# Optimization experiments

Measured on AMD Instinct MI355X. Metric: run time of the kernel, lower is better.

## Reference

```python
import jax, jax.numpy as jnp
import numpy as np

NUM_HEADS = 16
D_K = 8  # == n_qubits


def setup_inputs() -> dict:
    key = jax.random.key(0)
    k1, k2, k3 = jax.random.split(key, 3)
    x = jax.random.normal(k1, (4, 2048, 128), dtype=jnp.float32)
    # trainable RX angles, one per qubit (tq.RX has_params=True)
    theta = jax.random.normal(k2, (D_K,), dtype=jnp.float32)
    # out_proj: Linear(embed_dim, embed_dim, bias=False)
    w_out = jax.random.normal(k3, (128, 128), dtype=jnp.float32) * (1.0 / np.sqrt(128.0))
    return {"x": x, "theta": theta, "w_out": w_out}


def quantum_features(x, theta):
    # x: [b, s, e]. Per head of size d_k: encode RX(x_i), trainable RX(theta_i)
    # (composes to RX(x_i + theta_i)), CNOT ladder [i, i+1], measure PauliZ.
    # Heisenberg picture: Z_w -> Z_0...Z_w, so <Z_w> = prod_{i<=w} cos(x_i + theta_i).
    b, s, e = x.shape
    heads = x.reshape(b, s, NUM_HEADS, D_K)
    return jnp.cumprod(jnp.cos(heads + theta), axis=-1)  # [b, s, h, d_k]


def reference(x, theta, w_out):
    b, s, e = x.shape
    # q == k == v: same shared q_layer applied to the same x three times.
    qkv = quantum_features(x, theta)            # [b, s, h, d_k]
    q = qkv.transpose(0, 2, 1, 3)               # [b, h, s, d_k]
    scores = jnp.einsum('bhqd,bhkd->bhqk', q, q) / np.sqrt(D_K)
    attn = jax.nn.softmax(scores, axis=-1)      # dropout is identity at eval
    out = jnp.einsum('bhqk,bhkd->bhqd', attn, q)
    out = out.transpose(0, 2, 1, 3).reshape(b, s, e)
    return out @ w_out.T
```

## Files before the change

kernel.cpp:

```cpp
#include <hip/hip_runtime.h>

#define BATCH 4
#define SEQ   2048
#define EMB   128
#define NH    16
#define DK    8

#define QSCALE 0.510069726f

typedef _Float16 v2h __attribute__((ext_vector_type(2)));
typedef _Float16 v4h __attribute__((ext_vector_type(4)));
typedef __fp16   v2fp __attribute__((ext_vector_type(2)));
typedef float    v4f __attribute__((ext_vector_type(4)));

#define CHUNK  512
#define NCHUNK (SEQ / CHUNK)
#define VTP    520

__launch_bounds__(512, 8)
__global__ void attn_kernel(const float* __restrict__ x,
                            const float* __restrict__ theta,
                            _Float16* __restrict__ Ah ) {
  __shared__ __align__(16) _Float16 Kl[CHUNK * 8];
  __shared__ __align__(16) _Float16 VT[16][VTP];

  const int tid  = threadIdx.x;
  const int L    = tid & 63;
  const int quad = L >> 4;
  const int ln   = L & 15;
  const int wv   = tid >> 6;
  const int bh     = blockIdx.x >> 4;
  const int qchunk = blockIdx.x & 15;
  const int qb     = qchunk * 128 + wv * 16;
  const int b = bh >> 4;
  const int h = bh & 15;

  float th[DK];
#pragma unroll
  for (int i = 0; i < DK; ++i) th[i] = theta[i];

  for (int i = tid; i < 8 * VTP / 4; i += 512) {
    v4h v = (i < VTP / 4) ? (v4h){(_Float16)1.f, (_Float16)1.f,
                                  (_Float16)1.f, (_Float16)1.f}
                          : (v4h){0, 0, 0, 0};
    *(v4h*)(&VT[8][0] + i * 4) = v;
  }

  const int c0 = qchunk >> 2;
  v4h qf = {0, 0, 0, 0};
  v4f acc = (v4f){0.f, 0.f, 0.f, 0.f};
  const v4f zf = (v4f){0.f, 0.f, 0.f, 0.f};

  for (int cc = 0; cc < NCHUNK; ++cc) {
    const int c = (c0 + cc) & (NCHUNK - 1);
    if (cc) __syncthreads();

    {
      const float* xp = x + ((size_t)b * SEQ + c * CHUNK + tid) * EMB + h * DK;
      const float4 a0 = *(const float4*)(xp);
      const float4 a1 = *(const float4*)(xp + 4);

      float r[8];
      r[0] = __cosf(a0.x + th[0]);
      r[1] = r[0] * __cosf(a0.y + th[1]);
      r[2] = r[1] * __cosf(a0.z + th[2]);
      r[3] = r[2] * __cosf(a0.w + th[3]);
      r[4] = r[3] * __cosf(a1.x + th[4]);
      r[5] = r[4] * __cosf(a1.y + th[5]);
      r[6] = r[5] * __cosf(a1.z + th[6]);
      r[7] = r[6] * __cosf(a1.w + th[7]);

      _Float16 hv[8];
#pragma unroll
      for (int i = 0; i < 8; ++i) hv[i] = (_Float16)r[i];

      union { v4h v[2]; float4 f; } u;
      u.v[0] = (v4h){hv[0], hv[1], hv[2], hv[3]};
      u.v[1] = (v4h){hv[4], hv[5], hv[6], hv[7]};
      *(float4*)&Kl[tid * 8] = u.f;

#pragma unroll
      for (int d = 0; d < 8; ++d) VT[d][tid] = hv[d];
    }
    __syncthreads();

    if (cc == 0) {
      const v4h qsc = {(_Float16)QSCALE, (_Float16)QSCALE,
                       (_Float16)QSCALE, (_Float16)QSCALE};
      const int lrow = qb - c0 * CHUNK + ln;
      if (quad < 2) qf = *(const v4h*)&Kl[lrow * 8 + quad * 4] * qsc;
    }

    for (int t16 = 0; t16 < CHUNK / 16; ++t16) {
      const v4h kv = *(const v4h*)&Kl[(t16 * 16 + ln) * 8 + (quad & 1) * 4];
      const v4h kf = (quad < 2) ? kv : (v4h){0, 0, 0, 0};
      const v4h vt = *(const v4h*)&VT[ln][t16 * 16 + quad * 4];
      const v4f s = __builtin_amdgcn_mfma_f32_16x16x16f16(kf, qf, zf, 0, 0, 0);
      union { v2fp p[2]; v4h v; } pk;
      pk.p[0] = __builtin_amdgcn_cvt_pkrtz(__builtin_amdgcn_exp2f(s[0]),
                                           __builtin_amdgcn_exp2f(s[1]));
      pk.p[1] = __builtin_amdgcn_cvt_pkrtz(__builtin_amdgcn_exp2f(s[2]),
                                           __builtin_amdgcn_exp2f(s[3]));
      acc = __builtin_amdgcn_mfma_f32_16x16x16f16(vt, pk.v, acc, 0, 0, 0);
    }
  }

  {
    const float den = __shfl(acc[0], 32 + ln, 64);
    const float inv = 1.0f / den;
    if (quad < 2) {
      const int qrow = qb + ln;
      v4h o = {(_Float16)(acc[0] * inv), (_Float16)(acc[1] * inv),
               (_Float16)(acc[2] * inv), (_Float16)(acc[3] * inv)};
      *(v4h*)(Ah + ((size_t)b * SEQ + qrow) * EMB + h * DK + quad * 4) = o;
    }
  }
}

__launch_bounds__(256, 4)
__global__ void proj_kernel(const _Float16* __restrict__ Ah,
                            const float* __restrict__ W,
                            float* __restrict__ out) {
  __shared__ __align__(16) _Float16 Ahs[64][136];
  __shared__ __align__(16) _Float16 Whs[64][136];

  const int tid  = threadIdx.x;
  const int L    = tid & 63;
  const int wv   = tid >> 6;
  const int quad = L >> 4;
  const int ln   = L & 15;
  const int rowbase = blockIdx.x * 64;
  const int colbase = blockIdx.y * 64;

#pragma unroll
  for (int it = 0; it < 4; ++it) {
    const int idx = it * 256 + tid;
    const int r  = idx >> 4;
    const int c8 = idx & 15;
    *(uint4*)&Ahs[r][c8 * 8] =
        *(const uint4*)(Ah + (size_t)(rowbase + r) * EMB + c8 * 8);
  }
#pragma unroll
  for (int it = 0; it < 8; ++it) {
    const int idx = it * 256 + tid;
    const int n  = idx >> 5;
    const int c4 = idx & 31;
    const float4 w = *(const float4*)(W + (size_t)(colbase + n) * EMB + c4 * 4);
    v4h wh = {(_Float16)w.x, (_Float16)w.y, (_Float16)w.z, (_Float16)w.w};
    *(v4h*)&Whs[n][c4 * 4] = wh;
  }
  __syncthreads();

  v4f acc[4];
#pragma unroll
  for (int nt = 0; nt < 4; ++nt) acc[nt] = (v4f){0.f, 0.f, 0.f, 0.f};

#pragma unroll
  for (int k8 = 0; k8 < 8; ++k8) {
    const v4h af = *(const v4h*)&Ahs[wv * 16 + ln][k8 * 16 + quad * 4];
#pragma unroll
    for (int nt = 0; nt < 4; ++nt) {
      const v4h bf = *(const v4h*)&Whs[nt * 16 + ln][k8 * 16 + quad * 4];
      acc[nt] = __builtin_amdgcn_mfma_f32_16x16x16f16(af, bf, acc[nt], 0, 0, 0);
    }
  }

#pragma unroll
  for (int nt = 0; nt < 4; ++nt) {
    const int col = colbase + nt * 16 + ln;
#pragma unroll
    for (int r = 0; r < 4; ++r) {
      out[(size_t)(rowbase + wv * 16 + quad * 4 + r) * EMB + col] = acc[nt][r];
    }
  }
}

extern "C" void kernel_launch(void* const* d_in, const int* in_sizes, int n_in,
                              void* d_out, int out_size, void* d_ws, size_t ws_size,
                              hipStream_t stream) {
  const float* x     = (const float*)d_in[0];
  const float* theta = (const float*)d_in[1];
  const float* w_out = (const float*)d_in[2];
  float* out = (float*)d_out;

  _Float16* Ah = (_Float16*)d_ws;

  attn_kernel<<<dim3(1024), dim3(512), 0, stream>>>(x, theta, Ah);

  proj_kernel<<<dim3((BATCH * SEQ) / 64, 2), dim3(256), 0, stream>>>(Ah, w_out, out);
}
```

Baseline: 95.92 us.

## Split attention key range across two blocks with partial-sum reduce kernel

The attention kernel now splits the key sequence into two halves, each handled by a separate 256-thread block. Each wave processes two 16-row query tiles so that K/V fragments are reused, and the next chunk's x is prefetched into registers while the current chunk is computed. Unnormalised partial numerators and denominators are written in fp32 to a workspace, and a new reduce kernel combines the two halves and normalises before the projection. This adds an extra launch and extra global traffic in exchange for more blocks and better MFMA reuse per key load.

```diff
diff --git a/kernel.cpp b/kernel.cpp
--- a/kernel.cpp
+++ b/kernel.cpp
@@ -13,25 +13,29 @@
 typedef __fp16   v2fp __attribute__((ext_vector_type(2)));
 typedef float    v4f __attribute__((ext_vector_type(4)));
 
-#define CHUNK  512
-#define NCHUNK (SEQ / CHUNK)
-#define VTP    520
-
-__launch_bounds__(512, 8)
+#define CHUNK  256
+#define NCH    4
+#define VTPAD  264
+#define NROW   (BATCH * SEQ)
+#define NHROW  (BATCH * NH * SEQ)
+#define PSTR   12
+
+__launch_bounds__(256, 8)
 __global__ void attn_kernel(const float* __restrict__ x,
                             const float* __restrict__ theta,
-                            _Float16* __restrict__ Ah ) {
+                            float* __restrict__ Pp ) {
   __shared__ __align__(16) _Float16 Kl[CHUNK * 8];
-  __shared__ __align__(16) _Float16 VT[16][VTP];
+  __shared__ __align__(16) _Float16 VT[16][VTPAD];
 
   const int tid  = threadIdx.x;
   const int L    = tid & 63;
   const int quad = L >> 4;
   const int ln   = L & 15;
   const int wv   = tid >> 6;
-  const int bh     = blockIdx.x >> 4;
-  const int qchunk = blockIdx.x & 15;
-  const int qb     = qchunk * 128 + wv * 16;
+  const int bh     = blockIdx.x >> 5;
+  const int qchunk = (blockIdx.x >> 1) & 15;
+  const int split  = blockIdx.x & 1;
+  const int qb     = qchunk * 128 + wv * 32;
   const int b = bh >> 4;
   const int h = bh & 15;
 
@@ -39,27 +43,21 @@
 #pragma unroll
   for (int i = 0; i < DK; ++i) th[i] = theta[i];
 
-  for (int i = tid; i < 8 * VTP / 4; i += 512) {
-    v4h v = (i < VTP / 4) ? (v4h){(_Float16)1.f, (_Float16)1.f,
-                                  (_Float16)1.f, (_Float16)1.f}
-                          : (v4h){0, 0, 0, 0};
+  for (int i = tid; i < 8 * VTPAD / 4; i += 256) {
+    v4h v = (i < VTPAD / 4) ? (v4h){(_Float16)1.f, (_Float16)1.f,
+                                    (_Float16)1.f, (_Float16)1.f}
+                            : (v4h){0, 0, 0, 0};
     *(v4h*)(&VT[8][0] + i * 4) = v;
   }
 
-  const int c0 = qchunk >> 2;
-  v4h qf = {0, 0, 0, 0};
-  v4f acc = (v4f){0.f, 0.f, 0.f, 0.f};
-  const v4f zf = (v4f){0.f, 0.f, 0.f, 0.f};
-
-  for (int cc = 0; cc < NCHUNK; ++cc) {
-    const int c = (c0 + cc) & (NCHUNK - 1);
-    if (cc) __syncthreads();
-
-    {
-      const float* xp = x + ((size_t)b * SEQ + c * CHUNK + tid) * EMB + h * DK;
-      const float4 a0 = *(const float4*)(xp);
-      const float4 a1 = *(const float4*)(xp + 4);
-
+  v4h qf[2] = {{0, 0, 0, 0}, {0, 0, 0, 0}};
+  if (quad < 2) {
+#pragma unroll
+    for (int t = 0; t < 2; ++t) {
+      const int qrow = qb + t * 16 + ln;
+      const float* xq = x + ((size_t)b * SEQ + qrow) * EMB + h * DK;
+      const float4 a0 = *(const float4*)(xq);
+      const float4 a1 = *(const float4*)(xq + 4);
       float r[8];
       r[0] = __cosf(a0.x + th[0]);
       r[1] = r[0] * __cosf(a0.y + th[1]);
@@ -69,52 +67,109 @@
       r[5] = r[4] * __cosf(a1.y + th[5]);
       r[6] = r[5] * __cosf(a1.z + th[6]);
       r[7] = r[6] * __cosf(a1.w + th[7]);
-
+      qf[t] = (v4h){(_Float16)(r[quad * 4 + 0] * QSCALE),
+                    (_Float16)(r[quad * 4 + 1] * QSCALE),
+                    (_Float16)(r[quad * 4 + 2] * QSCALE),
+                    (_Float16)(r[quad * 4 + 3] * QSCALE)};
+    }
+  }
+
+  const float* xb = x + (size_t)b * SEQ * EMB + h * DK;
+  const int cbase = split * NCH;
+  float4 pa0, pa1;
+  {
+    const float* xp = xb + (size_t)(cbase * CHUNK + tid) * EMB;
+    pa0 = *(const float4*)(xp);
+    pa1 = *(const float4*)(xp + 4);
+  }
+
+  v4f acc[2];
+  acc[0] = (v4f){0.f, 0.f, 0.f, 0.f};
+  acc[1] = (v4f){0.f, 0.f, 0.f, 0.f};
+  const v4f zf = (v4f){0.f, 0.f, 0.f, 0.f};
+
+  for (int cc = 0; cc < NCH; ++cc) {
+    {
+      float r[8];
+      r[0] = __cosf(pa0.x + th[0]);
+      r[1] = r[0] * __cosf(pa0.y + th[1]);
+      r[2] = r[1] * __cosf(pa0.z + th[2]);
+      r[3] = r[2] * __cosf(pa0.w + th[3]);
+      r[4] = r[3] * __cosf(pa1.x + th[4]);
+      r[5] = r[4] * __cosf(pa1.y + th[5]);
+      r[6] = r[5] * __cosf(pa1.z + th[6]);
+      r[7] = r[6] * __cosf(pa1.w + th[7]);
       _Float16 hv[8];
 #pragma unroll
       for (int i = 0; i < 8; ++i) hv[i] = (_Float16)r[i];
-
       union { v4h v[2]; float4 f; } u;
       u.v[0] = (v4h){hv[0], hv[1], hv[2], hv[3]};
       u.v[1] = (v4h){hv[4], hv[5], hv[6], hv[7]};
       *(float4*)&Kl[tid * 8] = u.f;
-
 #pragma unroll
       for (int d = 0; d < 8; ++d) VT[d][tid] = hv[d];
     }
     __syncthreads();
 
-    if (cc == 0) {
-      const v4h qsc = {(_Float16)QSCALE, (_Float16)QSCALE,
-                       (_Float16)QSCALE, (_Float16)QSCALE};
-      const int lrow = qb - c0 * CHUNK + ln;
-      if (quad < 2) qf = *(const v4h*)&Kl[lrow * 8 + quad * 4] * qsc;
+    if (cc + 1 < NCH) {
+      const float* xp = xb + (size_t)((cbase + cc + 1) * CHUNK + tid) * EMB;
+      pa0 = *(const float4*)(xp);
+      pa1 = *(const float4*)(xp + 4);
     }
 
     for (int t16 = 0; t16 < CHUNK / 16; ++t16) {
-      const v4h kv = *(const v4h*)&Kl[(t16 * 16 + ln) * 8 + (quad & 1) * 4];
-      const v4h kf = (quad < 2) ? kv : (v4h){0, 0, 0, 0};
+      const v4h kf = *(const v4h*)&Kl[(t16 * 16 + ln) * 8 + (quad & 1) * 4];
       const v4h vt = *(const v4h*)&VT[ln][t16 * 16 + quad * 4];
-      const v4f s = __builtin_amdgcn_mfma_f32_16x16x16f16(kf, qf, zf, 0, 0, 0);
-      union { v2fp p[2]; v4h v; } pk;
-      pk.p[0] = __builtin_amdgcn_cvt_pkrtz(__builtin_amdgcn_exp2f(s[0]),
-                                           __builtin_amdgcn_exp2f(s[1]));
-      pk.p[1] = __builtin_amdgcn_cvt_pkrtz(__builtin_amdgcn_exp2f(s[2]),
-                                           __builtin_amdgcn_exp2f(s[3]));
-      acc = __builtin_amdgcn_mfma_f32_16x16x16f16(vt, pk.v, acc, 0, 0, 0);
-    }
-  }
-
-  {
-    const float den = __shfl(acc[0], 32 + ln, 64);
-    const float inv = 1.0f / den;
+#pragma unroll
+      for (int t = 0; t < 2; ++t) {
+        const v4f s = __builtin_amdgcn_mfma_f32_16x16x16f16(kf, qf[t], zf, 0, 0, 0);
+        union { v2fp p[2]; v4h v; } pk;
+        pk.p[0] = __builtin_amdgcn_cvt_pkrtz(__builtin_amdgcn_exp2f(s[0]),
+                                             __builtin_amdgcn_exp2f(s[1]));
+        pk.p[1] = __builtin_amdgcn_cvt_pkrtz(__builtin_amdgcn_exp2f(s[2]),
+                                             __builtin_amdgcn_exp2f(s[3]));
+        acc[t] = __builtin_amdgcn_mfma_f32_16x16x16f16(vt, pk.v, acc[t], 0, 0, 0);
+      }
+    }
+    __syncthreads();
+  }
+
+  float* pb = Pp + ((size_t)split * NHROW + (size_t)bh * SEQ) * PSTR;
+#pragma unroll
+  for (int t = 0; t < 2; ++t) {
+    const int qrow = qb + t * 16 + ln;
     if (quad < 2) {
-      const int qrow = qb + ln;
-      v4h o = {(_Float16)(acc[0] * inv), (_Float16)(acc[1] * inv),
-               (_Float16)(acc[2] * inv), (_Float16)(acc[3] * inv)};
-      *(v4h*)(Ah + ((size_t)b * SEQ + qrow) * EMB + h * DK + quad * 4) = o;
-    }
-  }
+      float4 st = make_float4(acc[t][0], acc[t][1], acc[t][2], acc[t][3]);
+      *(float4*)(pb + (size_t)qrow * PSTR + quad * 4) = st;
+    } else if (quad == 2) {
+      pb[(size_t)qrow * PSTR + 8] = acc[t][0];
+    }
+  }
+}
+
+__global__ void reduce_kernel(const float* __restrict__ Pp,
+                              _Float16* __restrict__ Ah) {
+  const int gid = blockIdx.x * 256 + threadIdx.x;
+  const int row = gid >> 4;
+  const int h   = gid & 15;
+  const int b   = row >> 11;
+  const int s   = row & (SEQ - 1);
+  const size_t pidx = ((size_t)(b * NH + h) * SEQ + s) * PSTR;
+
+  const float* p0 = Pp + pidx;
+  const float* p1 = Pp + (size_t)NHROW * PSTR + pidx;
+  const float4 a0 = *(const float4*)(p0);
+  const float4 a1 = *(const float4*)(p0 + 4);
+  const float4 b0 = *(const float4*)(p1);
+  const float4 b1 = *(const float4*)(p1 + 4);
+  const float inv = 1.0f / (p0[8] + p1[8]);
+
+  union { v4h v[2]; float4 f; } o;
+  o.v[0] = (v4h){(_Float16)((a0.x + b0.x) * inv), (_Float16)((a0.y + b0.y) * inv),
+                 (_Float16)((a0.z + b0.z) * inv), (_Float16)((a0.w + b0.w) * inv)};
+  o.v[1] = (v4h){(_Float16)((a1.x + b1.x) * inv), (_Float16)((a1.y + b1.y) * inv),
+                 (_Float16)((a1.z + b1.z) * inv), (_Float16)((a1.w + b1.w) * inv)};
+  *(float4*)(Ah + (size_t)row * EMB + h * DK) = o.f;
 }
 
 __launch_bounds__(256, 4)
@@ -184,8 +239,11 @@
   float* out = (float*)d_out;
 
   _Float16* Ah = (_Float16*)d_ws;
-
-  attn_kernel<<<dim3(1024), dim3(512), 0, stream>>>(x, theta, Ah);
-
-  proj_kernel<<<dim3((BATCH * SEQ) / 64, 2), dim3(256), 0, stream>>>(Ah, w_out, out);
-}
+  float*    Pp = (float*)((char*)d_ws + (size_t)4 * 1024 * 1024);
+
+  attn_kernel<<<dim3(2048), dim3(256), 0, stream>>>(x, theta, Pp);
+
+  reduce_kernel<<<dim3(512), dim3(256), 0, stream>>>(Pp, Ah);
+
+  proj_kernel<<<dim3(NROW / 64, 2), dim3(256), 0, stream>>>(Ah, w_out, out);
+}
```

Result: slower. 101.7 us (+6.0%).
